# Kernel optimization log

Measured on AMD Instinct MI355X. Metric: run time of the kernel, lower is better.

The kernel has to match this reference:

```python
import jax, jax.numpy as jnp
import numpy as np

ALPHA = 0.2          # LeakyReLU slope
NEG_BIG = -9e15      # mask value from the torch code
LN_EPS = 1e-5        # torch LayerNorm default eps
GAT_SCALE = 1.0


def _layer_norm(x, g, b):
    mu = x.mean(-1, keepdims=True)
    var = ((x - mu) ** 2).mean(-1, keepdims=True)
    return (x - mu) * jax.lax.rsqrt(var + LN_EPS) * g + b


def _gat_layer(h, adj, W, a, concat):
    # h: [B,N,Fin], adj: [N,N] weighted, W: [Fin,Fout], a: [2*Fout,1]
    Wh = jnp.einsum('bnf,fo->bno', h, W)                 # [B,N,Fout]
    Fo = W.shape[1]
    a_i, a_j = a[:Fo, 0], a[Fo:, 0]
    # e[b,i,j] = leakyrelu(Wh[b,i].a_i + Wh[b,j].a_j)  (== cat([Wh_i,Wh_j]) @ a)
    e = jax.nn.leaky_relu(
        (Wh @ a_i)[:, :, None] + (Wh @ a_j)[:, None, :], ALPHA)  # [B,N,N]
    att = jnp.where(adj[None, :, :] > 0, e, NEG_BIG)
    att = jax.nn.softmax(att, axis=2)
    att = att * adj[None, :, :]
    att = att / (att.sum(axis=2, keepdims=True) + 1e-8)
    h_prime = jnp.einsum('bij,bjo->bio', att, Wh)        # [B,N,Fout]
    return jax.nn.elu(h_prime) if concat else h_prime


def setup_inputs() -> dict:
    B, N, H, ID = 1024, 128, 64, 8
    GIN = 1 + ID  # node_feat_dim = 0
    key = jax.random.key(0)
    ks = jax.random.split(key, 20)
    # sparse weighted adjacency with self-loops
    w = jax.random.uniform(ks[0], (N, N))
    m = (jax.random.uniform(ks[1], (N, N)) < 0.3).astype(jnp.float32)
    adj = w * m + jnp.eye(N, dtype=jnp.float32)
    sc = lambda k, s: jax.random.normal(k, s, jnp.float32) * 0.1
    return {
        'c_values': jax.random.normal(ks[2], (B, N), jnp.float32),
        'adj': adj,
        'agent_emb': sc(ks[3], (N, ID)),
        'W1': sc(ks[4], (GIN, H)), 'a1': sc(ks[5], (2 * H, 1)),
        'W2': sc(ks[6], (H, H)),   'a2': sc(ks[7], (2 * H, 1)),
        'ln1_g': jnp.ones((H,)), 'ln1_b': jnp.zeros((H,)),
        'ln2_g': jnp.ones((H,)), 'ln2_b': jnp.zeros((H,)),
        'head_gat_w': sc(ks[8], (H, 1)), 'head_gat_b': jnp.zeros((1,)),
        'mlp1_w': sc(ks[9], (N, H)),  'mlp1_b': jnp.zeros((H,)),
        'mlp2_w': sc(ks[10], (H, H)), 'mlp2_b': jnp.zeros((H,)),
        'head_mlp_w': sc(ks[11], (H, 1)), 'head_mlp_b': jnp.zeros((1,)),
        'gate1_w': sc(ks[12], (N, H)), 'gate1_b': jnp.zeros((H,)),
        'gate2_w': sc(ks[13], (H, 1)), 'gate2_b': jnp.full((1,), -5.0),
    }


def reference(c_values, adj, agent_emb, W1, a1, W2, a2,
              ln1_g, ln1_b, ln2_g, ln2_b, head_gat_w, head_gat_b,
              mlp1_w, mlp1_b, mlp2_w, mlp2_b, head_mlp_w, head_mlp_b,
              gate1_w, gate1_b, gate2_w, gate2_b):
    B, N = c_values.shape
    # node features: [c_value, agent_id_embedding]
    id_feat = jnp.broadcast_to(agent_emb[None], (B, N, agent_emb.shape[1]))
    x_g = jnp.concatenate([c_values[..., None], id_feat], axis=-1)  # [B,N,9]
    h1 = _gat_layer(x_g, adj, W1, a1, concat=True)
    h1 = _layer_norm(h1, ln1_g, ln1_b)
    h2 = _gat_layer(h1, adj, W2, a2, concat=False)
    h = jax.nn.relu(h2 + h1)
    h = _layer_norm(h, ln2_g, ln2_b)
    q_gat = h.mean(axis=1) @ head_gat_w + head_gat_b                # [B,1]
    x_m = jax.nn.relu(c_values @ mlp1_w + mlp1_b)
    x_m = jax.nn.relu(x_m @ mlp2_w + mlp2_b)
    q_mlp = x_m @ head_mlp_w + head_mlp_b                           # [B,1]
    gate = jax.nn.sigmoid(
        jax.nn.relu(c_values @ gate1_w + gate1_b) @ gate2_w + gate2_b)
    return q_mlp + gate * GAT_SCALE * q_gat
```

## Files before the change

### kernel.cpp

```cpp
#include <hip/hip_runtime.h>
#include <hip/hip_bf16.h>

typedef unsigned short u16;
typedef unsigned int u32;
typedef short v8s __attribute__((ext_vector_type(8)));
typedef float v4f __attribute__((ext_vector_type(4)));

__device__ __forceinline__ float bflo(u32 d){union{u32 i;float f;}u;u.i=d<<16;return u.f;}
__device__ __forceinline__ float bfhi(u32 d){union{u32 i;float f;}u;u.i=d&0xffff0000u;return u.f;}
__device__ __forceinline__ u32 cvtpk(float a, float b){
    __hip_bfloat162 h = __float22bfloat162_rn(make_float2(a, b));
    u32 r; __builtin_memcpy(&r, &h, sizeof(r)); return r;
}
__device__ __forceinline__ v8s pack8(const float* w){
    union { uint4 u; v8s v; } c;
    c.u.x = cvtpk(w[0],w[1]); c.u.y = cvtpk(w[2],w[3]);
    c.u.z = cvtpk(w[4],w[5]); c.u.w = cvtpk(w[6],w[7]);
    return c.v;
}

__device__ __forceinline__ void flash_att(
    int wv, int l15, int q4,
    const float* __restrict__ ADJ,
    const float* __restrict__ sEi, const float* __restrict__ sFi,
    const float* __restrict__ sEj, const float* __restrict__ sFj,
    const u16* __restrict__ sWhT,
    v4f acc[2][4], v4f accD[2])
{
    const int r0 = 16*wv + l15, r1 = r0 + 64;
    const float Ei0 = sEi[r0], Fi0 = sFi[r0];
    const float Ei1 = sEi[r1], Fi1 = sFi[r1];
    const v8s ONES = {16256,16256,16256,16256,16256,16256,16256,16256};
    #pragma unroll
    for (int s = 0; s < 2; ++s) {
        accD[s] = (v4f){0.f,0.f,0.f,0.f};
        #pragma unroll
        for (int ct = 0; ct < 4; ++ct) acc[s][ct] = (v4f){0.f,0.f,0.f,0.f};
    }

    for (int ks = 0; ks < 4; ++ks) {
        const int ko = ks*32 + q4*8;
        float w0[8], w1[8];
        #pragma unroll
        for (int half = 0; half < 2; ++half) {
            float4 E4 = *(const float4*)(sEj + ko + 4*half);
            float4 F4 = *(const float4*)(sFj + ko + 4*half);
            float4 a0 = *(const float4*)(ADJ + r0*128 + ko + 4*half);
            float4 a1 = *(const float4*)(ADJ + r1*128 + ko + 4*half);
            float Ev[4] = {E4.x,E4.y,E4.z,E4.w};
            float Fv[4] = {F4.x,F4.y,F4.z,F4.w};
            float av0[4] = {a0.x,a0.y,a0.z,a0.w};
            float av1[4] = {a1.x,a1.y,a1.z,a1.w};
            #pragma unroll
            for (int k = 0; k < 4; ++k) {
                w0[half*4 + k] = fmaxf(Ei0*Ev[k], Fi0*Fv[k]) * av0[k];
                w1[half*4 + k] = fmaxf(Ei1*Ev[k], Fi1*Fv[k]) * av1[k];
            }
        }
        v8s A0 = pack8(w0), A1 = pack8(w1);
        accD[0] = __builtin_amdgcn_mfma_f32_16x16x32_bf16(ONES, A0, accD[0], 0,0,0);
        accD[1] = __builtin_amdgcn_mfma_f32_16x16x32_bf16(ONES, A1, accD[1], 0,0,0);
        #pragma unroll
        for (int ct = 0; ct < 4; ++ct) {
            v8s Wt = *(const v8s*)(sWhT + (16*ct + l15)*136 + ko);
            acc[0][ct] = __builtin_amdgcn_mfma_f32_16x16x32_bf16(Wt, A0, acc[0][ct], 0,0,0);
            acc[1][ct] = __builtin_amdgcn_mfma_f32_16x16x32_bf16(Wt, A1, acc[1][ct], 0,0,0);
        }
    }
}

__global__ __launch_bounds__(256, 4) void graphmixer_kernel(
    const float* __restrict__ C,
    const float* __restrict__ ADJ,
    const float* __restrict__ EMB,
    const float* __restrict__ W1,
    const float* __restrict__ A1,
    const float* __restrict__ W2,
    const float* __restrict__ A2,
    const float* __restrict__ LN1G, const float* __restrict__ LN1B,
    const float* __restrict__ LN2G, const float* __restrict__ LN2B,
    const float* __restrict__ HGW,  const float* __restrict__ HGB,
    const float* __restrict__ MLP1W, const float* __restrict__ MLP1B,
    const float* __restrict__ MLP2W, const float* __restrict__ MLP2B,
    const float* __restrict__ HMW,  const float* __restrict__ HMB,
    const float* __restrict__ G1W,  const float* __restrict__ G1B,
    const float* __restrict__ G2W,  const float* __restrict__ G2B,
    float* __restrict__ OUT)
{
    const int b = blockIdx.x, t = threadIdx.x;
    const int lane = t & 63, wv = t >> 6;
    const int l15 = lane & 15, q4 = lane >> 4;

    __shared__ __align__(16) unsigned char smem[40096];
    u16*   sWhT = (u16*)(smem);
    u16*   sH1  = (u16*)(smem + 17408);
    float* sEi  = (float*)(smem + 35840);
    float* sFi  = (float*)(smem + 36352);
    float* sEj  = (float*)(smem + 36864);
    float* sFj  = (float*)(smem + 37376);
    float* colp = (float*)(smem + 37888);
    float* sScr = (float*)(smem + 38912);
    float* v2i  = (float*)(smem + 39456);
    float* v2j  = (float*)(smem + 39712);
    float* v1i  = (float*)(smem + 39968);
    float* v1j  = (float*)(smem + 40032);
    float* sEmb = (float*)(smem + 17408);
    float* sC   = (float*)(smem + 21504);

    const float* Cb = C + b*128;

    if (wv == 0) {
        #pragma unroll
        for (int q = 0; q < 4; ++q)
            ((float4*)sEmb)[lane + 64*q] = ((const float4*)EMB)[lane + 64*q];
        if (lane < 32) ((float4*)sC)[lane] = ((const float4*)Cb)[lane];
        if (lane >= 32 && lane < 41) {
            int f = lane - 32; float a0 = 0.f, a1 = 0.f;
            for (int q = 0; q < 16; q += 2) {
                float4 w = *(const float4*)(W1 + f*64 + q*4);
                float4 x = *(const float4*)(A1 + q*4);
                a0 += w.x*x.x + w.y*x.y + w.z*x.z + w.w*x.w;
                float4 w2 = *(const float4*)(W1 + f*64 + (q+1)*4);
                float4 x2 = *(const float4*)(A1 + (q+1)*4);
                a1 += w2.x*x2.x + w2.y*x2.y + w2.z*x2.z + w2.w*x2.w;
            }
            v1i[f] = a0 + a1;
        } else if (lane >= 48 && lane < 57) {
            int f = lane - 48; float a0 = 0.f, a1 = 0.f;
            for (int q = 0; q < 16; q += 2) {
                float4 w = *(const float4*)(W1 + f*64 + q*4);
                float4 x = *(const float4*)(A1 + 64 + q*4);
                a0 += w.x*x.x + w.y*x.y + w.z*x.z + w.w*x.w;
                float4 w2 = *(const float4*)(W1 + f*64 + (q+1)*4);
                float4 x2 = *(const float4*)(A1 + 64 + (q+1)*4);
                a1 += w2.x*x2.x + w2.y*x2.y + w2.z*x2.z + w2.w*x2.w;
            }
            v1j[f] = a0 + a1;
        }
    } else if (wv == 3) {
        float ai0 = 0.f, ai1 = 0.f, aj0 = 0.f, aj1 = 0.f;
        for (int q = 0; q < 16; ++q) {
            float4 w  = *(const float4*)(W2 + lane*64 + q*4);
            float4 xi = *(const float4*)(A2 + q*4);
            float4 xj = *(const float4*)(A2 + 64 + q*4);
            ai0 += w.x*xi.x + w.y*xi.y; ai1 += w.z*xi.z + w.w*xi.w;
            aj0 += w.x*xj.x + w.y*xj.y; aj1 += w.z*xj.z + w.w*xj.w;
        }
        v2i[lane] = ai0 + ai1; v2j[lane] = aj0 + aj1;
    } else if (wv == 1) {
        float a0 = 0.f, a1 = 0.f, a2v = 0.f, a3 = 0.f;
        for (int k = 0; k < 128; k += 4) {
            float4 c4 = *(const float4*)(Cb + k);
            a0  += c4.x*MLP1W[k*64+lane];
            a1  += c4.y*MLP1W[(k+1)*64+lane];
            a2v += c4.z*MLP1W[(k+2)*64+lane];
            a3  += c4.w*MLP1W[(k+3)*64+lane];
        }
        sScr[lane] = fmaxf(a0+a1+a2v+a3 + MLP1B[lane], 0.f);
        float b0 = 0.f, b1 = 0.f, b2 = 0.f, b3 = 0.f;
        for (int k = 0; k < 64; k += 4) {
            b0 += sScr[k]  *MLP2W[k*64 + lane];
            b1 += sScr[k+1]*MLP2W[(k+1)*64 + lane];
            b2 += sScr[k+2]*MLP2W[(k+2)*64 + lane];
            b3 += sScr[k+3]*MLP2W[(k+3)*64 + lane];
        }
        float x2 = fmaxf(b0+b1+b2+b3 + MLP2B[lane], 0.f);
        float p1 = x2 * HMW[lane];
        #pragma unroll
        for (int off = 32; off >= 1; off >>= 1) p1 += __shfl_down(p1, off);
        if (lane == 0) sScr[128] = p1 + HMB[0];
    } else {
        float a0 = 0.f, a1 = 0.f, a2v = 0.f, a3 = 0.f;
        for (int k = 0; k < 128; k += 4) {
            float4 c4 = *(const float4*)(Cb + k);
            a0  += c4.x*G1W[k*64+lane];
            a1  += c4.y*G1W[(k+1)*64+lane];
            a2v += c4.z*G1W[(k+2)*64+lane];
            a3  += c4.w*G1W[(k+3)*64+lane];
        }
        float g1 = fmaxf(a0+a1+a2v+a3 + G1B[lane], 0.f);
        float p2 = g1 * G2W[lane];
        #pragma unroll
        for (int off = 32; off >= 1; off >>= 1) p2 += __shfl_down(p2, off);
        if (lane == 0) sScr[129] = 1.f / (1.f + __expf(-(p2 + G2B[0])));
    }
    __syncthreads();

    {
        const int o = lane, cc = wv;
        float w1f[9];
        #pragma unroll
        for (int f = 0; f < 9; ++f) w1f[f] = W1[f*64 + o];
        float whv[32];
        for (int i = 0; i < 32; ++i) {
            const int ig = cc*32 + i;
            float a = sC[ig] * w1f[0];
            float4 e0 = *(const float4*)(sEmb + ig*8);
            float4 e1 = *(const float4*)(sEmb + ig*8 + 4);
            a += e0.x*w1f[1] + e0.y*w1f[2] + e0.z*w1f[3] + e0.w*w1f[4];
            a += e1.x*w1f[5] + e1.y*w1f[6] + e1.z*w1f[7] + e1.w*w1f[8];
            whv[i] = a;
        }
        u32 p[16];
        #pragma unroll
        for (int q = 0; q < 16; ++q) p[q] = cvtpk(whv[2*q], whv[2*q+1]);
        uint4* dst = (uint4*)(sWhT + o*136 + cc*32);
        dst[0] = ((uint4*)p)[0]; dst[1] = ((uint4*)p)[1];
        dst[2] = ((uint4*)p)[2]; dst[3] = ((uint4*)p)[3];
    }
    if (t < 128) {
        float c = sC[t];
        float4 e0 = *(const float4*)(sEmb + t*8);
        float4 e1 = *(const float4*)(sEmb + t*8 + 4);
        float ei = c*v1i[0] + e0.x*v1i[1]+e0.y*v1i[2]+e0.z*v1i[3]+e0.w*v1i[4]
                            + e1.x*v1i[5]+e1.y*v1i[6]+e1.z*v1i[7]+e1.w*v1i[8];
        float ej = c*v1j[0] + e0.x*v1j[1]+e0.y*v1j[2]+e0.z*v1j[3]+e0.w*v1j[4]
                            + e1.x*v1j[5]+e1.y*v1j[6]+e1.z*v1j[7]+e1.w*v1j[8];
        sEi[t] = __expf(ei); sFi[t] = __expf(0.2f*ei);
        sEj[t] = __expf(ej); sFj[t] = __expf(0.2f*ej);
    }
    __syncthreads();

    uint2 h1p[2][4];
    float e2i[2], e2j[2];

    {
        v4f acc[2][4]; v4f accD[2];
        flash_att(wv, l15, q4, ADJ, sEi, sFi, sEj, sFj, sWhT, acc, accD);

        float4 g4[4], b4[4], vi4[4], vj4[4];
        #pragma unroll
        for (int ct = 0; ct < 4; ++ct) {
            g4[ct] = *(const float4*)(LN1G + 16*ct + 4*q4);
            b4[ct] = *(const float4*)(LN1B + 16*ct + 4*q4);
            vi4[ct] = *(const float4*)(v2i + 16*ct + 4*q4);
            vj4[ct] = *(const float4*)(v2j + 16*ct + 4*q4);
        }
        #pragma unroll
        for (int s = 0; s < 2; ++s) {
            const int row = 16*wv + l15 + 64*s;
            const float rd = 1.f / accD[s][0];
            float x[4][4]; float s1 = 0.f, s2 = 0.f;
            #pragma unroll
            for (int ct = 0; ct < 4; ++ct) {
                #pragma unroll
                for (int reg = 0; reg < 4; ++reg) {
                    float v = acc[s][ct][reg] * rd;
                    v = (v > 0.f) ? v : (__expf(v) - 1.f);
                    x[ct][reg] = v;
                }
                s1 += (x[ct][0]+x[ct][1]) + (x[ct][2]+x[ct][3]);
                s2 += (x[ct][0]*x[ct][0]+x[ct][1]*x[ct][1])
                    + (x[ct][2]*x[ct][2]+x[ct][3]*x[ct][3]);
            }
            s1 += __shfl_xor(s1, 16); s2 += __shfl_xor(s2, 16);
            s1 += __shfl_xor(s1, 32); s2 += __shfl_xor(s2, 32);
            const float mean = s1 * (1.f/64.f);
            const float var  = s2 * (1.f/64.f) - mean*mean;
            const float rstd = rsqrtf(var + 1e-5f);
            float ei = 0.f, ej = 0.f;
            #pragma unroll
            for (int ct = 0; ct < 4; ++ct) {
                float h0 = (x[ct][0] - mean) * rstd * g4[ct].x + b4[ct].x;
                float h1 = (x[ct][1] - mean) * rstd * g4[ct].y + b4[ct].y;
                float h2 = (x[ct][2] - mean) * rstd * g4[ct].z + b4[ct].z;
                float h3 = (x[ct][3] - mean) * rstd * g4[ct].w + b4[ct].w;
                uint2 pw; pw.x = cvtpk(h0, h1); pw.y = cvtpk(h2, h3);
                h1p[s][ct] = pw;
                *(uint2*)(sH1 + row*72 + 16*ct + 4*q4) = pw;
                ei += h0*vi4[ct].x + h1*vi4[ct].y + h2*vi4[ct].z + h3*vi4[ct].w;
                ej += h0*vj4[ct].x + h1*vj4[ct].y + h2*vj4[ct].z + h3*vj4[ct].w;
            }
            ei += __shfl_xor(ei, 16); ei += __shfl_xor(ei, 32);
            ej += __shfl_xor(ej, 16); ej += __shfl_xor(ej, 32);
            e2i[s] = ei; e2j[s] = ej;
        }
    }
    __syncthreads();

    if (q4 == 0) {
        #pragma unroll
        for (int s = 0; s < 2; ++s) {
            const int row = 16*wv + l15 + 64*s;
            sEi[row] = __expf(e2i[s]); sFi[row] = __expf(0.2f*e2i[s]);
            sEj[row] = __expf(e2j[s]); sFj[row] = __expf(0.2f*e2j[s]);
        }
    }

    {
        v4f acc2[2][4];
        #pragma unroll
        for (int s = 0; s < 2; ++s)
            #pragma unroll
            for (int ct = 0; ct < 4; ++ct) acc2[s][ct] = (v4f){0.f,0.f,0.f,0.f};
        #pragma unroll
        for (int ks = 0; ks < 2; ++ks) {
            const int kb = ks*32 + q4*8;
            v8s Bf[4];
            #pragma unroll
            for (int ct = 0; ct < 4; ++ct) {
                const float* wp = W2 + kb*64 + 16*ct + l15;
                float w8[8];
                #pragma unroll
                for (int j = 0; j < 8; ++j) w8[j] = wp[j*64];
                Bf[ct] = pack8(w8);
            }
            #pragma unroll
            for (int s = 0; s < 2; ++s) {
                v8s A = *(const v8s*)(sH1 + (16*(wv+4*s) + l15)*72 + kb);
                #pragma unroll
                for (int ct = 0; ct < 4; ++ct)
                    acc2[s][ct] = __builtin_amdgcn_mfma_f32_16x16x32_bf16(A, Bf[ct], acc2[s][ct], 0,0,0);
            }
        }
        #pragma unroll
        for (int s = 0; s < 2; ++s) {
            const int rb = 16*(wv+4*s) + 4*q4;
            #pragma unroll
            for (int ct = 0; ct < 4; ++ct) {
                const int col = 16*ct + l15;
                uint2 p;
                p.x = cvtpk(acc2[s][ct][0], acc2[s][ct][1]);
                p.y = cvtpk(acc2[s][ct][2], acc2[s][ct][3]);
                *(uint2*)(sWhT + col*136 + rb) = p;
            }
        }
    }
    __syncthreads();

    {
        v4f acc[2][4]; v4f accD[2];
        flash_att(wv, l15, q4, ADJ, sEi, sFi, sEj, sFj, sWhT, acc, accD);

        float4 g4[4], b4[4], hg4[4];
        #pragma unroll
        for (int ct = 0; ct < 4; ++ct) {
            g4[ct] = *(const float4*)(LN2G + 16*ct + 4*q4);
            b4[ct] = *(const float4*)(LN2B + 16*ct + 4*q4);
            hg4[ct] = *(const float4*)(HGW + 16*ct + 4*q4);
        }
        float ptot = 0.f;
        #pragma unroll
        for (int s = 0; s < 2; ++s) {
            const float rd = 1.f / accD[s][0];
            float x[4][4]; float s1 = 0.f, s2 = 0.f;
            #pragma unroll
            for (int ct = 0; ct < 4; ++ct) {
                const uint2 pw = h1p[s][ct];
                const float hv[4] = {bflo(pw.x), bfhi(pw.x), bflo(pw.y), bfhi(pw.y)};
                #pragma unroll
                for (int reg = 0; reg < 4; ++reg)
                    x[ct][reg] = fmaxf(acc[s][ct][reg] * rd + hv[reg], 0.f);
                s1 += (x[ct][0]+x[ct][1]) + (x[ct][2]+x[ct][3]);
                s2 += (x[ct][0]*x[ct][0]+x[ct][1]*x[ct][1])
                    + (x[ct][2]*x[ct][2]+x[ct][3]*x[ct][3]);
            }
            s1 += __shfl_xor(s1, 16); s2 += __shfl_xor(s2, 16);
            s1 += __shfl_xor(s1, 32); s2 += __shfl_xor(s2, 32);
            const float mean = s1 * (1.f/64.f);
            const float var  = s2 * (1.f/64.f) - mean*mean;
            const float rstd = rsqrtf(var + 1e-5f);
            #pragma unroll
            for (int ct = 0; ct < 4; ++ct) {
                float y0 = (x[ct][0] - mean) * rstd * g4[ct].x + b4[ct].x;
                float y1 = (x[ct][1] - mean) * rstd * g4[ct].y + b4[ct].y;
                float y2 = (x[ct][2] - mean) * rstd * g4[ct].z + b4[ct].z;
                float y3 = (x[ct][3] - mean) * rstd * g4[ct].w + b4[ct].w;
                ptot += y0*hg4[ct].x + y1*hg4[ct].y + y2*hg4[ct].z + y3*hg4[ct].w;
            }
        }
        ptot += __shfl_xor(ptot, 1);  ptot += __shfl_xor(ptot, 2);
        ptot += __shfl_xor(ptot, 4);  ptot += __shfl_xor(ptot, 8);
        ptot += __shfl_xor(ptot, 16); ptot += __shfl_xor(ptot, 32);
        if (lane == 0) colp[wv] = ptot;
    }
    __syncthreads();

    if (t == 0) {
        float s4 = (colp[0] + colp[1]) + (colp[2] + colp[3]);
        OUT[b] = sScr[128] + sScr[129] * (s4 * (1.f/128.f) + HGB[0]);
    }
}

extern "C" void kernel_launch(void* const* d_in, const int* in_sizes, int n_in,
                              void* d_out, int out_size, void* d_ws, size_t ws_size,
                              hipStream_t stream) {
    (void)n_in; (void)out_size; (void)d_ws; (void)ws_size;
    const float* C     = (const float*)d_in[0];
    const float* ADJ   = (const float*)d_in[1];
    const float* EMB   = (const float*)d_in[2];
    const float* W1    = (const float*)d_in[3];
    const float* A1    = (const float*)d_in[4];
    const float* W2    = (const float*)d_in[5];
    const float* A2    = (const float*)d_in[6];
    const float* LN1G  = (const float*)d_in[7];
    const float* LN1B  = (const float*)d_in[8];
    const float* LN2G  = (const float*)d_in[9];
    const float* LN2B  = (const float*)d_in[10];
    const float* HGW   = (const float*)d_in[11];
    const float* HGB   = (const float*)d_in[12];
    const float* MLP1W = (const float*)d_in[13];
    const float* MLP1B = (const float*)d_in[14];
    const float* MLP2W = (const float*)d_in[15];
    const float* MLP2B = (const float*)d_in[16];
    const float* HMW   = (const float*)d_in[17];
    const float* HMB   = (const float*)d_in[18];
    const float* G1W   = (const float*)d_in[19];
    const float* G1B   = (const float*)d_in[20];
    const float* G2W   = (const float*)d_in[21];
    const float* G2B   = (const float*)d_in[22];

    const int B = in_sizes[0] / 128;

    graphmixer_kernel<<<dim3(B), dim3(256), 0, stream>>>(
        C, ADJ, EMB, W1, A1, W2, A2, LN1G, LN1B, LN2G, LN2B,
        HGW, HGB, MLP1W, MLP1B, MLP2W, MLP2B, HMW, HMB,
        G1W, G1B, G2W, G2B, (float*)d_out);
}
```

Baseline: 132.8 us.

## Alias shared buffers to shrink LDS and raise occupancy target to seven blocks

```diff
diff --git a/kernel.cpp b/kernel.cpp
--- a/kernel.cpp
+++ b/kernel.cpp
@@ -69,7 +69,7 @@
     }
 }
 
-__global__ __launch_bounds__(256, 4) void graphmixer_kernel(
+__global__ __launch_bounds__(256, 7) void graphmixer_kernel(
     const float* __restrict__ C,
     const float* __restrict__ ADJ,
     const float* __restrict__ EMB,
@@ -91,29 +91,23 @@
     const int lane = t & 63, wv = t >> 6;
     const int l15 = lane & 15, q4 = lane >> 4;
 
-    __shared__ __align__(16) unsigned char smem[40096];
+    __shared__ __align__(16) unsigned char smem[21712];
     u16*   sWhT = (u16*)(smem);
-    u16*   sH1  = (u16*)(smem + 17408);
-    float* sEi  = (float*)(smem + 35840);
-    float* sFi  = (float*)(smem + 36352);
-    float* sEj  = (float*)(smem + 36864);
-    float* sFj  = (float*)(smem + 37376);
-    float* colp = (float*)(smem + 37888);
-    float* sScr = (float*)(smem + 38912);
-    float* v2i  = (float*)(smem + 39456);
-    float* v2j  = (float*)(smem + 39712);
-    float* v1i  = (float*)(smem + 39968);
-    float* v1j  = (float*)(smem + 40032);
-    float* sEmb = (float*)(smem + 17408);
-    float* sC   = (float*)(smem + 21504);
+    u16*   sH1  = (u16*)(smem);
+    float* sEi  = (float*)(smem + 18432);
+    float* sFi  = (float*)(smem + 18944);
+    float* sEj  = (float*)(smem + 19456);
+    float* sFj  = (float*)(smem + 19968);
+    float* sScr = (float*)(smem + 20480);
+    float* v2i  = (float*)(smem + 21056);
+    float* v2j  = (float*)(smem + 21312);
+    float* v1i  = (float*)(smem + 21568);
+    float* v1j  = (float*)(smem + 21632);
+    float* colp = (float*)(smem + 21696);
 
     const float* Cb = C + b*128;
 
     if (wv == 0) {
-        #pragma unroll
-        for (int q = 0; q < 4; ++q)
-            ((float4*)sEmb)[lane + 64*q] = ((const float4*)EMB)[lane + 64*q];
-        if (lane < 32) ((float4*)sC)[lane] = ((const float4*)Cb)[lane];
         if (lane >= 32 && lane < 41) {
             int f = lane - 32; float a0 = 0.f, a1 = 0.f;
             for (int q = 0; q < 16; q += 2) {
@@ -194,9 +188,9 @@
         float whv[32];
         for (int i = 0; i < 32; ++i) {
             const int ig = cc*32 + i;
-            float a = sC[ig] * w1f[0];
-            float4 e0 = *(const float4*)(sEmb + ig*8);
-            float4 e1 = *(const float4*)(sEmb + ig*8 + 4);
+            float a = Cb[ig] * w1f[0];
+            float4 e0 = *(const float4*)(EMB + ig*8);
+            float4 e1 = *(const float4*)(EMB + ig*8 + 4);
             a += e0.x*w1f[1] + e0.y*w1f[2] + e0.z*w1f[3] + e0.w*w1f[4];
             a += e1.x*w1f[5] + e1.y*w1f[6] + e1.z*w1f[7] + e1.w*w1f[8];
             whv[i] = a;
@@ -209,9 +203,9 @@
         dst[2] = ((uint4*)p)[2]; dst[3] = ((uint4*)p)[3];
     }
     if (t < 128) {
-        float c = sC[t];
-        float4 e0 = *(const float4*)(sEmb + t*8);
-        float4 e1 = *(const float4*)(sEmb + t*8 + 4);
+        float c = Cb[t];
+        float4 e0 = *(const float4*)(EMB + t*8);
+        float4 e1 = *(const float4*)(EMB + t*8 + 4);
         float ei = c*v1i[0] + e0.x*v1i[1]+e0.y*v1i[2]+e0.z*v1i[3]+e0.w*v1i[4]
                             + e1.x*v1i[5]+e1.y*v1i[6]+e1.z*v1i[7]+e1.w*v1i[8];
         float ej = c*v1j[0] + e0.x*v1j[1]+e0.y*v1j[2]+e0.z*v1j[3]+e0.w*v1j[4]
@@ -222,11 +216,11 @@
     __syncthreads();
 
     uint2 h1p[2][4];
-    float e2i[2], e2j[2];
 
     {
         v4f acc[2][4]; v4f accD[2];
         flash_att(wv, l15, q4, ADJ, sEi, sFi, sEj, sFj, sWhT, acc, accD);
+        __syncthreads();
 
         float4 g4[4], b4[4], vi4[4], vj4[4];
         #pragma unroll
@@ -273,21 +267,22 @@
             }
             ei += __shfl_xor(ei, 16); ei += __shfl_xor(ei, 32);
             ej += __shfl_xor(ej, 16); ej += __shfl_xor(ej, 32);
-            e2i[s] = ei; e2j[s] = ej;
+            if (q4 == 0) {
+                sEi[row] = __expf(ei); sFi[row] = __expf(0.2f*ei);
+                sEj[row] = __expf(ej); sFj[row] = __expf(0.2f*ej);
+            }
         }
     }
     __syncthreads();
 
-    if (q4 == 0) {
-        #pragma unroll
-        for (int s = 0; s < 2; ++s) {
-            const int row = 16*wv + l15 + 64*s;
-            sEi[row] = __expf(e2i[s]); sFi[row] = __expf(0.2f*e2i[s]);
-            sEj[row] = __expf(e2j[s]); sFj[row] = __expf(0.2f*e2j[s]);
-        }
-    }
-
     {
+        v8s Af[2][2];
+        #pragma unroll
+        for (int s = 0; s < 2; ++s)
+            #pragma unroll
+            for (int ks = 0; ks < 2; ++ks)
+                Af[s][ks] = *(const v8s*)(sH1 + (16*(wv+4*s) + l15)*72 + ks*32 + q4*8);
+
         v4f acc2[2][4];
         #pragma unroll
         for (int s = 0; s < 2; ++s)
@@ -296,23 +291,19 @@
         #pragma unroll
         for (int ks = 0; ks < 2; ++ks) {
             const int kb = ks*32 + q4*8;
-            v8s Bf[4];
             #pragma unroll
             for (int ct = 0; ct < 4; ++ct) {
                 const float* wp = W2 + kb*64 + 16*ct + l15;
                 float w8[8];
                 #pragma unroll
                 for (int j = 0; j < 8; ++j) w8[j] = wp[j*64];
-                Bf[ct] = pack8(w8);
-            }
-            #pragma unroll
-            for (int s = 0; s < 2; ++s) {
-                v8s A = *(const v8s*)(sH1 + (16*(wv+4*s) + l15)*72 + kb);
+                v8s Bf = pack8(w8);
                 #pragma unroll
-                for (int ct = 0; ct < 4; ++ct)
-                    acc2[s][ct] = __builtin_amdgcn_mfma_f32_16x16x32_bf16(A, Bf[ct], acc2[s][ct], 0,0,0);
-            }
-        }
+                for (int s = 0; s < 2; ++s)
+                    acc2[s][ct] = __builtin_amdgcn_mfma_f32_16x16x32_bf16(Af[s][ks], Bf, acc2[s][ct], 0,0,0);
+            }
+        }
+        __syncthreads();
         #pragma unroll
         for (int s = 0; s < 2; ++s) {
             const int rb = 16*(wv+4*s) + 4*q4;
```

After: 248.0 us. 86.8% more time.
